# Optimization experiments

Hardware: AMD Instinct MI355X
Metric: run time of the kernel (lower is better)

## Reference

```python
import jax, jax.numpy as jnp
import numpy as np
from jax import lax

EPS = 1e-5
DW_THRESH = 4.0
PW_THRESH = 1e-3


def setup_inputs() -> dict:
    key = jax.random.key(0)
    ks = jax.random.split(key, 13)
    B, C, O, H, W = 32, 256, 256, 56, 56
    inp = {
        "x": jax.random.normal(ks[0], (B, C, H, W), jnp.float32),
        "dw_w": jax.random.normal(ks[1], (C, 1, 3, 3), jnp.float32) * 0.2,
        "dw_b": jax.random.normal(ks[2], (C,), jnp.float32) * 0.1,
        "bn1_gamma": 0.5 + jax.random.uniform(ks[3], (C,), jnp.float32) * 1.5,
        "bn1_beta": jax.random.normal(ks[4], (C,), jnp.float32) * 0.5,
        "bn1_mean": jax.random.normal(ks[5], (C,), jnp.float32) * 0.1,
        "bn1_var": 0.5 + jax.random.uniform(ks[6], (C,), jnp.float32),
        "pw_w": jax.random.normal(ks[7], (O, C, 1, 1), jnp.float32) * 0.06,
        "pw_b": jax.random.normal(ks[8], (O,), jnp.float32) * 0.1,
        "bn2_gamma": 0.5 + jax.random.uniform(ks[9], (O,), jnp.float32) * 1.5,
        "bn2_beta": jax.random.normal(ks[10], (O,), jnp.float32) * 0.5,
        "bn2_mean": jax.random.normal(ks[11], (O,), jnp.float32) * 0.1,
        "bn2_var": 0.5 + jax.random.uniform(ks[12], (O,), jnp.float32),
    }
    return inp


def _bn(x, gamma, beta, mean, var):
    # inference-mode BatchNorm2d over channel axis 1
    inv = gamma * lax.rsqrt(var + EPS)
    return x * inv[None, :, None, None] + (beta - mean * inv)[None, :, None, None]


def _cut(x, thresh):
    # per-(batch, channel) max-abs pruning: max(max(x), -min(x)) == max(|x|)
    max_abs = jnp.max(jnp.abs(x), axis=(2, 3))  # [B, C]
    return jnp.where((max_abs < thresh)[:, :, None, None], 0.0, x)


def reference(x, dw_w, dw_b, bn1_gamma, bn1_beta, bn1_mean, bn1_var,
              pw_w, pw_b, bn2_gamma, bn2_beta, bn2_mean, bn2_var):
    C = x.shape[1]
    # depthwise 3x3 conv, padding=1, groups=C
    y = lax.conv_general_dilated(
        x, dw_w, window_strides=(1, 1), padding=[(1, 1), (1, 1)],
        feature_group_count=C,
        dimension_numbers=("NCHW", "OIHW", "NCHW"),
    ) + dw_b[None, :, None, None]
    y = jax.nn.relu(_bn(y, bn1_gamma, bn1_beta, bn1_mean, bn1_var))
    y = _cut(y, DW_THRESH)
    # pointwise 1x1 conv as channel contraction
    z = jnp.einsum("bihw,oi->bohw", y, pw_w[:, :, 0, 0]) + pw_b[None, :, None, None]
    z = jax.nn.relu(_bn(z, bn2_gamma, bn2_beta, bn2_mean, bn2_var))
    z = _cut(z, PW_THRESH)
    return z
```

## Files before the change

### kernel.cpp

```cpp
#include <hip/hip_runtime.h>
#include <hip/hip_bf16.h>
#include <stdint.h>

#define BATCH 32
#define CIN   256
#define COUT  256
#define HDIM  56
#define HW    3136
#define NPAD  3200

typedef short bf16x8 __attribute__((ext_vector_type(8)));
typedef float f32x4  __attribute__((ext_vector_type(4)));

__device__ __forceinline__ unsigned short f2bf(float f) {
    unsigned u = __float_as_uint(f);
    u += 0x7fffu + ((u >> 16) & 1u);
    return (unsigned short)(u >> 16);
}

__global__ __launch_bounds__(256) void prep_kernel(
        const float* __restrict__ pw_w, const float* __restrict__ pw_b,
        const float* __restrict__ g2, const float* __restrict__ be2,
        const float* __restrict__ mu2, const float* __restrict__ va2,
        unsigned short* __restrict__ Wp, float* __restrict__ b2,
        unsigned* __restrict__ pwmax) {
    int o = blockIdx.x;
    int t = threadIdx.x;
    float inv2 = g2[o] * rsqrtf(va2[o] + 1e-5f);
    Wp[o * CIN + t] = f2bf(pw_w[o * CIN + t] * inv2);
    if (t == 0) b2[o] = pw_b[o] * inv2 + be2[o] - mu2[o] * inv2;
    int idx = blockIdx.x * 256 + t;
    if (idx < BATCH * COUT) pwmax[idx] = 0u;
}

__global__ __launch_bounds__(256) void dw_kernel(
        const float* __restrict__ x, const float* __restrict__ dww,
        const float* __restrict__ dwb,
        const float* __restrict__ g1, const float* __restrict__ be1,
        const float* __restrict__ mu1, const float* __restrict__ va1,
        unsigned short* __restrict__ y) {
    int blk = blockIdx.x;
    int c = blk & 255;
    int b = blk >> 8;
    int tid = threadIdx.x;

    __shared__ float xs[58 * 58];
    __shared__ float red[4];
    __shared__ float bmax_sh;

    const float* xp = x + (size_t)(b * CIN + c) * HW;
    for (int idx = tid; idx < 58 * 58; idx += 256) {
        int r = idx / 58;
        int q = idx - r * 58;
        int gr = r - 1, gc = q - 1;
        float v = 0.f;
        if ((unsigned)gr < 56u && (unsigned)gc < 56u) v = xp[gr * 56 + gc];
        xs[idx] = v;
    }

    float w0 = dww[c * 9 + 0], w1 = dww[c * 9 + 1], w2 = dww[c * 9 + 2];
    float w3 = dww[c * 9 + 3], w4 = dww[c * 9 + 4], w5 = dww[c * 9 + 5];
    float w6 = dww[c * 9 + 6], w7 = dww[c * 9 + 7], w8 = dww[c * 9 + 8];
    float bias = dwb[c];
    float inv = g1[c] * rsqrtf(va1[c] + 1e-5f);
    float sh  = be1[c] - mu1[c] * inv;
    __syncthreads();

    float vals[13];
    float lmax = 0.f;
#pragma unroll
    for (int i = 0; i < 13; ++i) {
        int p = tid + i * 256;
        float v = 0.f;
        if (p < HW) {
            int h = p / 56;
            int w = p - h * 56;
            const float* bp = &xs[h * 58 + w];
            float a = bp[0] * w0 + bp[1] * w1 + bp[2] * w2
                    + bp[58] * w3 + bp[59] * w4 + bp[60] * w5
                    + bp[116] * w6 + bp[117] * w7 + bp[118] * w8;
            v = (a + bias) * inv + sh;
            v = fmaxf(v, 0.f);
            lmax = fmaxf(lmax, v);
        }
        vals[i] = v;
    }
    for (int off = 32; off >= 1; off >>= 1)
        lmax = fmaxf(lmax, __shfl_xor(lmax, off, 64));
    if ((tid & 63) == 0) red[tid >> 6] = lmax;
    __syncthreads();
    if (tid == 0) bmax_sh = fmaxf(fmaxf(red[0], red[1]), fmaxf(red[2], red[3]));
    __syncthreads();
    bool cut = (bmax_sh < 4.0f);

    unsigned short* yp = y + (size_t)(b * CIN + c) * NPAD;
#pragma unroll
    for (int i = 0; i < 13; ++i) {
        int p = tid + i * 256;
        if (p < HW) yp[p] = cut ? (unsigned short)0 : f2bf(vals[i]);
    }
    if (tid < NPAD - HW) yp[HW + tid] = 0;
}

#define MT 128
#define NT 128
#define KS 64

__global__ __launch_bounds__(256) void pw_kernel(
        const unsigned short* __restrict__ y, const unsigned short* __restrict__ Wp,
        const float* __restrict__ b2, float* __restrict__ z,
        unsigned* __restrict__ pwmax) {
    __shared__ __align__(16) unsigned short Al[MT * KS];
    __shared__ __align__(16) unsigned short Bl[NT * KS];

    int bid = blockIdx.x;
    int mt = bid & 1;
    int rest = bid >> 1;
    int nt = rest % 25;
    int b = rest / 25;
    int m0 = mt * 128, n0 = nt * 128;

    int tid = threadIdx.x;
    int lane = tid & 63, wid = tid >> 6;
    int wm = (wid & 1) * 64, wn = (wid >> 1) * 64;
    int l15 = lane & 15, l4 = lane >> 4;

    f32x4 acc[4][4];
#pragma unroll
    for (int mf = 0; mf < 4; ++mf)
#pragma unroll
        for (int nf = 0; nf < 4; ++nf) acc[mf][nf] = {0.f, 0.f, 0.f, 0.f};

    const unsigned short* yb = y + (size_t)b * CIN * NPAD;

    for (int kk = 0; kk < 4; ++kk) {
        int k0 = kk * 64;
        __syncthreads();
#pragma unroll
        for (int i = 0; i < 4; ++i) {
            int s = tid + i * 256;
            int m = s >> 3, cch = s & 7;
            int dch = cch ^ (m & 7);
            uint4 v = *(const uint4*)(Wp + (size_t)(m0 + m) * CIN + k0 + dch * 8);
            *(uint4*)((char*)Al + m * 128 + cch * 16) = v;
        }
#pragma unroll
        for (int i = 0; i < 2; ++i) {
            int u = tid + i * 256;
            int q = u >> 5, nq = u & 31;
            const unsigned short* src = yb + (size_t)(k0 + q * 4) * NPAD + n0 + nq * 4;
            uint2 r0 = *(const uint2*)(src);
            uint2 r1 = *(const uint2*)(src + NPAD);
            uint2 r2 = *(const uint2*)(src + 2 * NPAD);
            uint2 r3 = *(const uint2*)(src + 3 * NPAD);
#pragma unroll
            for (int i2 = 0; i2 < 4; ++i2) {
                unsigned x0 = (i2 & 2) ? r0.y : r0.x;
                unsigned x1 = (i2 & 2) ? r1.y : r1.x;
                unsigned x2 = (i2 & 2) ? r2.y : r2.x;
                unsigned x3 = (i2 & 2) ? r3.y : r3.x;
                if (i2 & 1) { x0 >>= 16; x2 >>= 16; }
                else        { x0 &= 0xffffu; x2 &= 0xffffu; }
                unsigned px = (i2 & 1) ? (x0 | (x1 & 0xffff0000u))
                                       : (x0 | (x1 << 16));
                unsigned py = (i2 & 1) ? (x2 | (x3 & 0xffff0000u))
                                       : (x2 | (x3 << 16));
                int nloc = nq * 4 + i2;
                int sb = nloc * 128 + (((q >> 1) ^ ((nloc >> 2) & 7)) << 4) + ((q & 1) << 3);
                *(uint2*)((char*)Bl + sb) = make_uint2(px, py);
            }
        }
        __syncthreads();
#pragma unroll
        for (int h = 0; h < 2; ++h) {
            bf16x8 af[4], bfr[4];
            int cc = h * 4 + l4;
#pragma unroll
            for (int mf = 0; mf < 4; ++mf) {
                int m = wm + mf * 16 + l15;
                af[mf] = *(const bf16x8*)((const char*)Al + m * 128 + ((cc ^ (m & 7)) << 4));
            }
#pragma unroll
            for (int nf = 0; nf < 4; ++nf) {
                int n = wn + nf * 16 + l15;
                bfr[nf] = *(const bf16x8*)((const char*)Bl + n * 128 + ((cc ^ ((n >> 2) & 7)) << 4));
            }
#pragma unroll
            for (int mf = 0; mf < 4; ++mf)
#pragma unroll
                for (int nf = 0; nf < 4; ++nf)
                    acc[mf][nf] = __builtin_amdgcn_mfma_f32_16x16x32_bf16(
                        af[mf], bfr[nf], acc[mf][nf], 0, 0, 0);
        }
    }

    float* zb = z + (size_t)b * COUT * HW;
#pragma unroll
    for (int mf = 0; mf < 4; ++mf) {
        int obase = m0 + wm + mf * 16 + l4 * 4;
        float bb0 = b2[obase + 0], bb1 = b2[obase + 1];
        float bb2v = b2[obase + 2], bb3 = b2[obase + 3];
        float rmax[4] = {0.f, 0.f, 0.f, 0.f};
#pragma unroll
        for (int nf = 0; nf < 4; ++nf) {
            int n = n0 + wn + nf * 16 + l15;
            bool valid = (n < HW);
            float v0 = fmaxf(acc[mf][nf][0] + bb0, 0.f);
            float v1 = fmaxf(acc[mf][nf][1] + bb1, 0.f);
            float v2 = fmaxf(acc[mf][nf][2] + bb2v, 0.f);
            float v3 = fmaxf(acc[mf][nf][3] + bb3, 0.f);
            if (valid) {
                zb[(size_t)(obase + 0) * HW + n] = v0;
                zb[(size_t)(obase + 1) * HW + n] = v1;
                zb[(size_t)(obase + 2) * HW + n] = v2;
                zb[(size_t)(obase + 3) * HW + n] = v3;
                rmax[0] = fmaxf(rmax[0], v0);
                rmax[1] = fmaxf(rmax[1], v1);
                rmax[2] = fmaxf(rmax[2], v2);
                rmax[3] = fmaxf(rmax[3], v3);
            }
        }
#pragma unroll
        for (int r = 0; r < 4; ++r) {
            float v = rmax[r];
            v = fmaxf(v, __shfl_xor(v, 1, 64));
            v = fmaxf(v, __shfl_xor(v, 2, 64));
            v = fmaxf(v, __shfl_xor(v, 4, 64));
            v = fmaxf(v, __shfl_xor(v, 8, 64));
            if (l15 == 0)
                atomicMax(&pwmax[b * COUT + obase + r], __float_as_uint(v));
        }
    }
}

__global__ __launch_bounds__(256) void cut_kernel(const unsigned* __restrict__ pwmax,
                                                  float* __restrict__ z) {
    int bo = blockIdx.x;
    if (__uint_as_float(pwmax[bo]) >= 1e-3f) return;
    float4* zp = (float4*)(z + (size_t)bo * HW);
    for (int i = threadIdx.x; i < HW / 4; i += 256)
        zp[i] = make_float4(0.f, 0.f, 0.f, 0.f);
}

extern "C" void kernel_launch(void* const* d_in, const int* in_sizes, int n_in,
                              void* d_out, int out_size, void* d_ws, size_t ws_size,
                              hipStream_t stream) {
    const float* x   = (const float*)d_in[0];
    const float* dww = (const float*)d_in[1];
    const float* dwb = (const float*)d_in[2];
    const float* g1  = (const float*)d_in[3];
    const float* be1 = (const float*)d_in[4];
    const float* mu1 = (const float*)d_in[5];
    const float* va1 = (const float*)d_in[6];
    const float* pww = (const float*)d_in[7];
    const float* pwb = (const float*)d_in[8];
    const float* g2  = (const float*)d_in[9];
    const float* be2 = (const float*)d_in[10];
    const float* mu2 = (const float*)d_in[11];
    const float* va2 = (const float*)d_in[12];
    float* z = (float*)d_out;

    char* ws = (char*)d_ws;
    const size_t Y_BYTES = (size_t)BATCH * CIN * NPAD * 2;
    unsigned short* y  = (unsigned short*)ws;
    unsigned short* Wp = (unsigned short*)(ws + Y_BYTES);
    float* b2          = (float*)(ws + Y_BYTES + 131072);
    unsigned* pwmax    = (unsigned*)(ws + Y_BYTES + 131072 + 1024);

    prep_kernel<<<256, 256, 0, stream>>>(pww, pwb, g2, be2, mu2, va2, Wp, b2, pwmax);
    dw_kernel<<<BATCH * CIN, 256, 0, stream>>>(x, dww, dwb, g1, be1, mu1, va1, y);
    pw_kernel<<<2 * 25 * BATCH, 256, 0, stream>>>(y, Wp, b2, z, pwmax);
    cut_kernel<<<BATCH * COUT, 256, 0, stream>>>(pwmax, z);
}
```

Measured before the change: 113.9 us.

## Register-tile depthwise conv, prefetch pointwise GEMM tiles, batch cut blocks

Result: slower. 121.0 us (+6.2%).

```diff
diff --git a/kernel.cpp b/kernel.cpp
--- a/kernel.cpp
+++ b/kernel.cpp
@@ -5,7 +5,6 @@
 #define BATCH 32
 #define CIN   256
 #define COUT  256
-#define HDIM  56
 #define HW    3136
 #define NPAD  3200
 
@@ -43,48 +42,55 @@
     int c = blk & 255;
     int b = blk >> 8;
     int tid = threadIdx.x;
-
-    __shared__ float xs[58 * 58];
+    const float* xp = x + (size_t)(b * CIN + c) * HW;
+
+    float w00 = dww[c*9+0], w01 = dww[c*9+1], w02 = dww[c*9+2];
+    float w10 = dww[c*9+3], w11 = dww[c*9+4], w12 = dww[c*9+5];
+    float w20 = dww[c*9+6], w21 = dww[c*9+7], w22 = dww[c*9+8];
+    float inv = g1[c] * rsqrtf(va1[c] + 1e-5f);
+    float b0  = dwb[c] * inv + (be1[c] - mu1[c] * inv);
+
+    float vals[4][4];
+    float lmax = 0.f;
+#pragma unroll
+    for (int i = 0; i < 4; ++i) {
+        int q = tid + i * 256;
+        int qq = q < 784 ? q : 783;
+        int h = qq / 14;
+        int c0 = (qq - h * 14) * 4;
+        float a0 = 0.f, a1 = 0.f, a2 = 0.f, a3 = 0.f;
+#pragma unroll
+        for (int r = 0; r < 3; ++r) {
+            int gr = h + r - 1;
+            bool rv = (unsigned)gr < 56u;
+            int grc = gr < 0 ? 0 : (gr > 55 ? 55 : gr);
+            const float* rowp = xp + grc * 56;
+            float4 vv = *(const float4*)(rowp + c0);
+            float s0 = (rv && c0 != 0) ? rowp[c0 - 1] : 0.f;
+            float s5 = (rv && c0 < 52) ? rowp[c0 + 4] : 0.f;
+            float s1 = rv ? vv.x : 0.f;
+            float s2 = rv ? vv.y : 0.f;
+            float s3 = rv ? vv.z : 0.f;
+            float s4 = rv ? vv.w : 0.f;
+            float wl = r == 0 ? w00 : (r == 1 ? w10 : w20);
+            float wc = r == 0 ? w01 : (r == 1 ? w11 : w21);
+            float wr = r == 0 ? w02 : (r == 1 ? w12 : w22);
+            a0 = fmaf(s0, wl, fmaf(s1, wc, fmaf(s2, wr, a0)));
+            a1 = fmaf(s1, wl, fmaf(s2, wc, fmaf(s3, wr, a1)));
+            a2 = fmaf(s2, wl, fmaf(s3, wc, fmaf(s4, wr, a2)));
+            a3 = fmaf(s3, wl, fmaf(s4, wc, fmaf(s5, wr, a3)));
+        }
+        float v0 = fmaxf(fmaf(a0, inv, b0), 0.f);
+        float v1 = fmaxf(fmaf(a1, inv, b0), 0.f);
+        float v2 = fmaxf(fmaf(a2, inv, b0), 0.f);
+        float v3 = fmaxf(fmaf(a3, inv, b0), 0.f);
+        vals[i][0] = v0; vals[i][1] = v1; vals[i][2] = v2; vals[i][3] = v3;
+        if (q < 784)
+            lmax = fmaxf(lmax, fmaxf(fmaxf(v0, v1), fmaxf(v2, v3)));
+    }
+
     __shared__ float red[4];
     __shared__ float bmax_sh;
-
-    const float* xp = x + (size_t)(b * CIN + c) * HW;
-    for (int idx = tid; idx < 58 * 58; idx += 256) {
-        int r = idx / 58;
-        int q = idx - r * 58;
-        int gr = r - 1, gc = q - 1;
-        float v = 0.f;
-        if ((unsigned)gr < 56u && (unsigned)gc < 56u) v = xp[gr * 56 + gc];
-        xs[idx] = v;
-    }
-
-    float w0 = dww[c * 9 + 0], w1 = dww[c * 9 + 1], w2 = dww[c * 9 + 2];
-    float w3 = dww[c * 9 + 3], w4 = dww[c * 9 + 4], w5 = dww[c * 9 + 5];
-    float w6 = dww[c * 9 + 6], w7 = dww[c * 9 + 7], w8 = dww[c * 9 + 8];
-    float bias = dwb[c];
-    float inv = g1[c] * rsqrtf(va1[c] + 1e-5f);
-    float sh  = be1[c] - mu1[c] * inv;
-    __syncthreads();
-
-    float vals[13];
-    float lmax = 0.f;
-#pragma unroll
-    for (int i = 0; i < 13; ++i) {
-        int p = tid + i * 256;
-        float v = 0.f;
-        if (p < HW) {
-            int h = p / 56;
-            int w = p - h * 56;
-            const float* bp = &xs[h * 58 + w];
-            float a = bp[0] * w0 + bp[1] * w1 + bp[2] * w2
-                    + bp[58] * w3 + bp[59] * w4 + bp[60] * w5
-                    + bp[116] * w6 + bp[117] * w7 + bp[118] * w8;
-            v = (a + bias) * inv + sh;
-            v = fmaxf(v, 0.f);
-            lmax = fmaxf(lmax, v);
-        }
-        vals[i] = v;
-    }
     for (int off = 32; off >= 1; off >>= 1)
         lmax = fmaxf(lmax, __shfl_xor(lmax, off, 64));
     if ((tid & 63) == 0) red[tid >> 6] = lmax;
@@ -94,24 +100,28 @@
     bool cut = (bmax_sh < 4.0f);
 
     unsigned short* yp = y + (size_t)(b * CIN + c) * NPAD;
-#pragma unroll
-    for (int i = 0; i < 13; ++i) {
-        int p = tid + i * 256;
-        if (p < HW) yp[p] = cut ? (unsigned short)0 : f2bf(vals[i]);
-    }
-    if (tid < NPAD - HW) yp[HW + tid] = 0;
-}
-
-#define MT 128
-#define NT 128
-#define KS 64
+    ushort4 zero4 = make_ushort4(0, 0, 0, 0);
+#pragma unroll
+    for (int i = 0; i < 4; ++i) {
+        int q = tid + i * 256;
+        if (q < 784) {
+            ushort4 o = zero4;
+            if (!cut) {
+                o.x = f2bf(vals[i][0]); o.y = f2bf(vals[i][1]);
+                o.z = f2bf(vals[i][2]); o.w = f2bf(vals[i][3]);
+            }
+            *(ushort4*)(yp + q * 4) = o;
+        }
+    }
+    if (tid < 16) *(ushort4*)(yp + HW + tid * 4) = zero4;
+}
 
 __global__ __launch_bounds__(256) void pw_kernel(
         const unsigned short* __restrict__ y, const unsigned short* __restrict__ Wp,
         const float* __restrict__ b2, float* __restrict__ z,
         unsigned* __restrict__ pwmax) {
-    __shared__ __align__(16) unsigned short Al[MT * KS];
-    __shared__ __align__(16) unsigned short Bl[NT * KS];
+    __shared__ __align__(16) unsigned short Al[128 * 64];
+    __shared__ __align__(16) unsigned short Bl[128 * 64];
 
     int bid = blockIdx.x;
     int mt = bid & 1;
@@ -125,34 +135,52 @@
     int wm = (wid & 1) * 64, wn = (wid >> 1) * 64;
     int l15 = lane & 15, l4 = lane >> 4;
 
+    const unsigned short* yb = y + (size_t)b * CIN * NPAD;
+
+    int am[4], acch[4];
+    const unsigned short* asrc[4];
+#pragma unroll
+    for (int i = 0; i < 4; ++i) {
+        int s = i * 256 + tid;
+        int m = s >> 3, cch = s & 7, dch = cch ^ (m & 7);
+        am[i] = m; acch[i] = cch;
+        asrc[i] = Wp + (size_t)(m0 + m) * CIN + dch * 8;
+    }
+    int bq[2], bnq[2];
+    const unsigned short* bsrc[2];
+#pragma unroll
+    for (int i = 0; i < 2; ++i) {
+        int u = tid + i * 256;
+        bq[i] = u >> 5; bnq[i] = u & 31;
+        bsrc[i] = yb + (size_t)(bq[i] * 4) * NPAD + n0 + bnq[i] * 4;
+    }
+
+    uint4 areg[4];
+    uint2 breg[2][4];
+#pragma unroll
+    for (int i = 0; i < 4; ++i) areg[i] = *(const uint4*)(asrc[i]);
+#pragma unroll
+    for (int i = 0; i < 2; ++i)
+#pragma unroll
+        for (int r = 0; r < 4; ++r) breg[i][r] = *(const uint2*)(bsrc[i] + r * NPAD);
+
     f32x4 acc[4][4];
 #pragma unroll
     for (int mf = 0; mf < 4; ++mf)
 #pragma unroll
         for (int nf = 0; nf < 4; ++nf) acc[mf][nf] = {0.f, 0.f, 0.f, 0.f};
 
-    const unsigned short* yb = y + (size_t)b * CIN * NPAD;
-
+#pragma unroll
     for (int kk = 0; kk < 4; ++kk) {
-        int k0 = kk * 64;
-        __syncthreads();
-#pragma unroll
-        for (int i = 0; i < 4; ++i) {
-            int s = tid + i * 256;
-            int m = s >> 3, cch = s & 7;
-            int dch = cch ^ (m & 7);
-            uint4 v = *(const uint4*)(Wp + (size_t)(m0 + m) * CIN + k0 + dch * 8);
-            *(uint4*)((char*)Al + m * 128 + cch * 16) = v;
-        }
+        __builtin_amdgcn_s_barrier();
+        __builtin_amdgcn_sched_barrier(0);
+#pragma unroll
+        for (int i = 0; i < 4; ++i)
+            *(uint4*)((char*)Al + am[i] * 128 + acch[i] * 16) = areg[i];
 #pragma unroll
         for (int i = 0; i < 2; ++i) {
-            int u = tid + i * 256;
-            int q = u >> 5, nq = u & 31;
-            const unsigned short* src = yb + (size_t)(k0 + q * 4) * NPAD + n0 + nq * 4;
-            uint2 r0 = *(const uint2*)(src);
-            uint2 r1 = *(const uint2*)(src + NPAD);
-            uint2 r2 = *(const uint2*)(src + 2 * NPAD);
-            uint2 r3 = *(const uint2*)(src + 3 * NPAD);
+            uint2 r0 = breg[i][0], r1 = breg[i][1], r2 = breg[i][2], r3 = breg[i][3];
+            int q = bq[i], nq = bnq[i];
 #pragma unroll
             for (int i2 = 0; i2 < 4; ++i2) {
                 unsigned x0 = (i2 & 2) ? r0.y : r0.x;
@@ -170,7 +198,19 @@
                 *(uint2*)((char*)Bl + sb) = make_uint2(px, py);
             }
         }
-        __syncthreads();
+        if (kk < 3) {
+#pragma unroll
+            for (int i = 0; i < 4; ++i)
+                areg[i] = *(const uint4*)(asrc[i] + (kk + 1) * 64);
+#pragma unroll
+            for (int i = 0; i < 2; ++i)
+#pragma unroll
+                for (int r = 0; r < 4; ++r)
+                    breg[i][r] = *(const uint2*)(bsrc[i] + (size_t)(kk + 1) * 64 * NPAD + r * NPAD);
+        }
+        asm volatile("s_waitcnt lgkmcnt(0)" ::: "memory");
+        __builtin_amdgcn_s_barrier();
+        __builtin_amdgcn_sched_barrier(0);
 #pragma unroll
         for (int h = 0; h < 2; ++h) {
             bf16x8 af[4], bfr[4];
@@ -235,11 +275,15 @@
 
 __global__ __launch_bounds__(256) void cut_kernel(const unsigned* __restrict__ pwmax,
                                                   float* __restrict__ z) {
-    int bo = blockIdx.x;
-    if (__uint_as_float(pwmax[bo]) >= 1e-3f) return;
-    float4* zp = (float4*)(z + (size_t)bo * HW);
-    for (int i = threadIdx.x; i < HW / 4; i += 256)
-        zp[i] = make_float4(0.f, 0.f, 0.f, 0.f);
+    int base = blockIdx.x * 8;
+#pragma unroll
+    for (int j = 0; j < 8; ++j) {
+        int bo = base + j;
+        if (__uint_as_float(pwmax[bo]) >= 1e-3f) continue;
+        float4* zp = (float4*)(z + (size_t)bo * HW);
+        for (int i = threadIdx.x; i < HW / 4; i += 256)
+            zp[i] = make_float4(0.f, 0.f, 0.f, 0.f);
+    }
 }
 
 extern "C" void kernel_launch(void* const* d_in, const int* in_sizes, int n_in,
@@ -270,5 +314,5 @@
     prep_kernel<<<256, 256, 0, stream>>>(pww, pwb, g2, be2, mu2, va2, Wp, b2, pwmax);
     dw_kernel<<<BATCH * CIN, 256, 0, stream>>>(x, dww, dwb, g1, be1, mu1, va1, y);
     pw_kernel<<<2 * 25 * BATCH, 256, 0, stream>>>(y, Wp, b2, z, pwmax);
-    cut_kernel<<<BATCH * COUT, 256, 0, stream>>>(pwmax, z);
-}
+    cut_kernel<<<BATCH * COUT / 8, 256, 0, stream>>>(pwmax, z);
+}
```
